# Optimization experiments

Measured on AMD Instinct MI355X. Metric: run time of the kernel, lower is better.

## Reference

```python
import jax, jax.numpy as jnp
import numpy as np
import math

N_EMBD = 1024
N_HEAD = 16
HEAD_DIM = N_EMBD // N_HEAD
SCALE = 1.0 / math.sqrt(HEAD_DIM)


def setup_inputs() -> dict:
    key = jax.random.key(0)
    ks = jax.random.split(key, 5)
    B, S = 1, 4096
    std = 0.02
    x = jax.random.normal(ks[0], (B, S, N_EMBD), dtype=jnp.float32)
    # Linear weights stored as [in, out] (transposed vs torch storage; same math)
    w_qkv = jax.random.normal(ks[1], (N_EMBD, 3 * N_EMBD), dtype=jnp.float32) * std
    b_qkv = jnp.zeros((3 * N_EMBD,), dtype=jnp.float32)
    w_out = jax.random.normal(ks[2], (N_EMBD, N_EMBD), dtype=jnp.float32) * std
    b_out = jnp.zeros((N_EMBD,), dtype=jnp.float32)
    return {"x": x, "w_qkv": w_qkv, "b_qkv": b_qkv, "w_out": w_out, "b_out": b_out}


def reference(x, w_qkv, b_qkv, w_out, b_out):
    B, S, D = x.shape
    qkv = x @ w_qkv + b_qkv                      # [B, S, 3D]
    q, k, v = jnp.split(qkv, 3, axis=-1)
    # [B, H, S, d]
    q = q.reshape(B, S, N_HEAD, HEAD_DIM).transpose(0, 2, 1, 3)
    k = k.reshape(B, S, N_HEAD, HEAD_DIM).transpose(0, 2, 1, 3)
    v = v.reshape(B, S, N_HEAD, HEAD_DIM).transpose(0, 2, 1, 3)
    scores = jnp.einsum("bhqd,bhkd->bhqk", q, k) * SCALE  # [B, H, S, S]
    causal = jnp.tril(jnp.ones((S, S), dtype=bool))
    scores = jnp.where(causal, scores, -jnp.inf)
    attn = jax.nn.softmax(scores, axis=-1)
    out = jnp.einsum("bhqk,bhkd->bhqd", attn, v)  # [B, H, S, d]
    out = out.transpose(0, 2, 1, 3).reshape(B, S, D)
    return out @ w_out + b_out
```

## Files before the change

### kernel.cpp

```cpp
#include <hip/hip_runtime.h>
#include <hip/hip_bf16.h>
#include <cstdint>

typedef __bf16 bf16x8 __attribute__((ext_vector_type(8)));
typedef float  f32x4  __attribute__((ext_vector_type(4)));

#define S_LEN 4096
#define D_EMB 1024
#define N3    3072
#define HDIM  64

__device__ __forceinline__ unsigned short f2bf(float f) {
    union { unsigned int i; float f; } v; v.f = f;
    unsigned int i = v.i;
    return (unsigned short)((i + 0x7FFFu + ((i >> 16) & 1u)) >> 16);
}

__device__ __forceinline__ void async16(const void* g, void* l) {
    __builtin_amdgcn_global_load_lds(
        (const __attribute__((address_space(1))) unsigned int*)g,
        (__attribute__((address_space(3))) unsigned int*)l,
        16, 0, 0);
}

__global__ void convert_f32_bf16(const float* __restrict__ src,
                                 unsigned short* __restrict__ dst, int n8) {
    const int i = blockIdx.x * blockDim.x + threadIdx.x;
    if (i >= n8) return;
    float4 f0 = *(const float4*)&src[i * 8];
    float4 f1 = *(const float4*)&src[i * 8 + 4];
    union { uint4 q; unsigned short s[8]; } o;
    o.s[0]=f2bf(f0.x); o.s[1]=f2bf(f0.y); o.s[2]=f2bf(f0.z); o.s[3]=f2bf(f0.w);
    o.s[4]=f2bf(f1.x); o.s[5]=f2bf(f1.y); o.s[6]=f2bf(f1.z); o.s[7]=f2bf(f1.w);
    *(uint4*)&dst[i * 8] = o.q;
}

__global__ void transpose_f32_to_bf16(const float* __restrict__ src,
                                      unsigned short* __restrict__ dst,
                                      int R, int ld, int c0) {
    __shared__ float tile[32][33];
    const int tx = threadIdx.x, ty = threadIdx.y;
    const int r0 = blockIdx.y * 32, cc0 = blockIdx.x * 32;
    for (int i = 0; i < 32; i += 8)
        tile[ty + i][tx] = src[(size_t)(r0 + ty + i) * ld + c0 + cc0 + tx];
    __syncthreads();
    for (int i = 0; i < 32; i += 8)
        dst[(size_t)(cc0 + ty + i) * R + r0 + tx] = f2bf(tile[tx][ty + i]);
}

template <int MI, bool OUT_F32, bool FUSE_VT>
__global__ __launch_bounds__(256) void gemm_bt_bias(
    const unsigned short* __restrict__ A,
    const unsigned short* __restrict__ BT,
    const float* __restrict__ bias,
    void* __restrict__ Cp,
    unsigned short* __restrict__ Vt,
    int M, int N, int K)
{
    constexpr int MTILE = MI * 32;
    constexpr int LA = MI / 2;
    __shared__ __align__(16) unsigned short As[MTILE * 32];
    __shared__ __align__(16) unsigned short Bs[128 * 32];
    const int tid  = threadIdx.x;
    const int wave = tid >> 6, lane = tid & 63;
    const int q4 = lane >> 4, l16 = lane & 15;
    const int m0 = blockIdx.y * MTILE, n0 = blockIdx.x * 128;
    const int wm = (wave >> 1) * (MI * 16), wn = (wave & 1) * 64;

    f32x4 acc[MI][4] = {};

    const int lrow = lane >> 2;
    const int scol = (lane & 3) * 8;

    for (int k0 = 0; k0 < K; k0 += 32) {
        __syncthreads();
        for (int i = 0; i < 2; ++i) {
            const int r = wave * 32 + i * 16 + lrow;
            async16(BT + (size_t)(n0 + r) * K + k0 + scol,
                    &Bs[(wave * 32 + i * 16) * 32 + lane * 8]);
        }
        for (int i = 0; i < LA; ++i) {
            const int r = wave * (16 * LA) + i * 16 + lrow;
            async16(A + (size_t)(m0 + r) * K + k0 + scol,
                    &As[(wave * (16 * LA) + i * 16) * 32 + lane * 8]);
        }
        __syncthreads();

        bf16x8 af[MI], bfr[4];
        for (int mi = 0; mi < MI; ++mi)
            af[mi] = *(const bf16x8*)&As[(wm + mi * 16 + l16) * 32 + q4 * 8];
        for (int ni = 0; ni < 4; ++ni)
            bfr[ni] = *(const bf16x8*)&Bs[(wn + ni * 16 + l16) * 32 + q4 * 8];
        for (int mi = 0; mi < MI; ++mi)
            for (int ni = 0; ni < 4; ++ni)
                acc[mi][ni] = __builtin_amdgcn_mfma_f32_16x16x32_bf16(
                    af[mi], bfr[ni], acc[mi][ni], 0, 0, 0);
    }

    if (FUSE_VT && n0 >= 2048) {
        for (int ni = 0; ni < 4; ++ni) {
            const int col = n0 + wn + ni * 16 + l16;
            const float bv = bias[col];
            const int vrow = col - 2048;
            for (int mi = 0; mi < MI; ++mi) {
                const int row = m0 + wm + mi * 16 + q4 * 4;
                union { uint2 u; unsigned short s[4]; } pk;
                for (int r = 0; r < 4; ++r) pk.s[r] = f2bf(acc[mi][ni][r] + bv);
                *(uint2*)&Vt[(size_t)vrow * S_LEN + row] = pk.u;
            }
        }
        return;
    }
    for (int ni = 0; ni < 4; ++ni) {
        const int col = n0 + wn + ni * 16 + l16;
        const float bv = bias[col];
        for (int mi = 0; mi < MI; ++mi) {
            const int row = m0 + wm + mi * 16 + q4 * 4;
            for (int r = 0; r < 4; ++r) {
                const float val = acc[mi][ni][r] + bv;
                if constexpr (OUT_F32)
                    ((float*)Cp)[(size_t)(row + r) * N + col] = val;
                else
                    ((unsigned short*)Cp)[(size_t)(row + r) * N + col] = f2bf(val);
            }
        }
    }
}

#define LDP 72
#define EXP2_SCALE 0.180336884f

__global__ __launch_bounds__(256) void attn_flash(
    const unsigned short* __restrict__ qkv,
    const unsigned short* __restrict__ Vt,
    unsigned short* __restrict__ X2)
{
    __shared__ __align__(16) unsigned short Ks[64 * LDP];
    __shared__ __align__(16) unsigned short Vs[64 * LDP];
    __shared__ __align__(16) unsigned short Ps[4 * 16 * LDP];
    const int tid  = threadIdx.x;
    const int wave = tid >> 6, lane = tid & 63;
    const int q4 = lane >> 4, l16 = lane & 15;
    const int h  = blockIdx.y;

    const int x = blockIdx.x, hg = blockIdx.y >> 2;
    int qt;
    if      (hg == 0) qt = x;
    else if (hg == 1) qt = 63 - x;
    else if (hg == 2) qt = (x + 16) & 63;
    else              qt = (47 - x) & 63;
    const int q0 = qt * 64;

    bf16x8 aq[2];
    {
        const unsigned short* qp =
            qkv + (size_t)(q0 + wave * 16 + l16) * N3 + h * HDIM + q4 * 8;
        aq[0] = *(const bf16x8*)(qp);
        aq[1] = *(const bf16x8*)(qp + 32);
    }

    float l_part[4] = {0.f, 0.f, 0.f, 0.f};
    f32x4 o[4] = {};

    const int rr = tid >> 3;
    const int cc = (tid & 7) * 8;
    unsigned short* Pw = &Ps[wave * 16 * LDP];

    for (int t = 0; t <= qt; ++t) {
        const int kv0 = t * 64;
        uint4 kv_a = *(const uint4*)&qkv[(size_t)(kv0 + rr)      * N3 + D_EMB + h * HDIM + cc];
        uint4 kv_b = *(const uint4*)&qkv[(size_t)(kv0 + 32 + rr) * N3 + D_EMB + h * HDIM + cc];
        uint4 vt_a = *(const uint4*)&Vt [(size_t)(h * HDIM + rr)      * S_LEN + kv0 + cc];
        uint4 vt_b = *(const uint4*)&Vt [(size_t)(h * HDIM + 32 + rr) * S_LEN + kv0 + cc];
        __syncthreads();
        *(uint4*)&Ks[rr * LDP + cc]        = kv_a;
        *(uint4*)&Ks[(32 + rr) * LDP + cc] = kv_b;
        *(uint4*)&Vs[rr * LDP + cc]        = vt_a;
        *(uint4*)&Vs[(32 + rr) * LDP + cc] = vt_b;
        __syncthreads();

        f32x4 sacc[4] = {};
        for (int kk = 0; kk < 2; ++kk)
            for (int nt = 0; nt < 4; ++nt) {
                bf16x8 b = *(const bf16x8*)&Ks[(nt * 16 + l16) * LDP + kk * 32 + q4 * 8];
                sacc[nt] = __builtin_amdgcn_mfma_f32_16x16x32_bf16(
                    aq[kk], b, sacc[nt], 0, 0, 0);
            }

        if (t < qt) {
            for (int r = 0; r < 4; ++r) {
                const int prow = (q4 * 4 + r) * LDP;
                for (int nt = 0; nt < 4; ++nt) {
                    float e = exp2f(sacc[nt][r] * EXP2_SCALE);
                    l_part[r] += e;
                    Pw[prow + nt * 16 + l16] =
                        (unsigned short)(__float_as_uint(e) >> 16);
                }
            }
        } else {
            for (int r = 0; r < 4; ++r) {
                const int grow = q0 + wave * 16 + q4 * 4 + r;
                const int prow = (q4 * 4 + r) * LDP;
                for (int nt = 0; nt < 4; ++nt) {
                    float e = exp2f(sacc[nt][r] * EXP2_SCALE);
                    if (kv0 + nt * 16 + l16 > grow) e = 0.f;
                    l_part[r] += e;
                    Pw[prow + nt * 16 + l16] =
                        (unsigned short)(__float_as_uint(e) >> 16);
                }
            }
        }
        __asm__ volatile("s_waitcnt lgkmcnt(0)" ::: "memory");

        for (int kk = 0; kk < 2; ++kk) {
            bf16x8 pa = *(const bf16x8*)&Pw[l16 * LDP + kk * 32 + q4 * 8];
            for (int dt = 0; dt < 4; ++dt) {
                bf16x8 vb = *(const bf16x8*)&Vs[(dt * 16 + l16) * LDP + kk * 32 + q4 * 8];
                o[dt] = __builtin_amdgcn_mfma_f32_16x16x32_bf16(pa, vb, o[dt], 0, 0, 0);
            }
        }
    }

    float linv[4];
    for (int r = 0; r < 4; ++r) {
        float l = l_part[r];
        for (int off = 1; off < 16; off <<= 1)
            l += __shfl_xor(l, off, 16);
        linv[r] = 1.f / l;
    }
    for (int dt = 0; dt < 4; ++dt)
        for (int r = 0; r < 4; ++r) {
            const int row = q0 + wave * 16 + q4 * 4 + r;
            X2[(size_t)row * D_EMB + h * HDIM + dt * 16 + l16] =
                f2bf(o[dt][r] * linv[r]);
        }
}

extern "C" void kernel_launch(void* const* d_in, const int* in_sizes, int n_in,
                              void* d_out, int out_size, void* d_ws, size_t ws_size,
                              hipStream_t stream) {
    const float* x     = (const float*)d_in[0];
    const float* w_qkv = (const float*)d_in[1];
    const float* b_qkv = (const float*)d_in[2];
    const float* w_out = (const float*)d_in[3];
    const float* b_out = (const float*)d_in[4];
    float* out = (float*)d_out;

    char* ws = (char*)d_ws;
    unsigned short* qkv   = (unsigned short*)(ws);
    unsigned short* wqkvT = (unsigned short*)(ws + 25165824);
    unsigned short* woutT = (unsigned short*)(ws + 31457280);
    unsigned short* Vt    = (unsigned short*)(ws + 33554432);
    unsigned short* X2    = (unsigned short*)(ws + 41943040);
    unsigned short* Xb    = X2;

    convert_f32_bf16<<<(4096 * 1024 / 8 + 255) / 256, 256, 0, stream>>>(
        x, Xb, 4096 * 1024 / 8);

    transpose_f32_to_bf16<<<dim3(3072 / 32, 1024 / 32), dim3(32, 8), 0, stream>>>(
        w_qkv, wqkvT, 1024, 3072, 0);
    transpose_f32_to_bf16<<<dim3(1024 / 32, 1024 / 32), dim3(32, 8), 0, stream>>>(
        w_out, woutT, 1024, 1024, 0);

    gemm_bt_bias<4, false, true><<<dim3(3072 / 128, 4096 / 128), 256, 0, stream>>>(
        Xb, wqkvT, b_qkv, qkv, Vt, 4096, 3072, 1024);

    attn_flash<<<dim3(64, 16), 256, 0, stream>>>(qkv, Vt, X2);

    gemm_bt_bias<2, true, false><<<dim3(1024 / 128, 4096 / 64), 256, 0, stream>>>(
        X2, woutT, b_out, out, nullptr, 4096, 1024, 1024);
}
```

Measured before the change: 251.6 us.

## Prefetch next K/V tile in registers, fold softmax scale into Q, split V transpose

The attention loop now loads the next K/V tile into registers right after the LDS store, so global loads overlap the QK and PV MFMAs of the current tile. The softmax scale times log2e is folded into the Q columns in the QKV GEMM epilogue, which removes one multiply per score. The fused V-transpose epilogue is dropped from the GEMM and replaced by a separate bf16 transpose kernel. That adds a kernel launch and an extra read and write of V in exchange for coalesced GEMM stores.

```diff
diff --git a/kernel.cpp b/kernel.cpp
--- a/kernel.cpp
+++ b/kernel.cpp
@@ -9,6 +9,7 @@
 #define D_EMB 1024
 #define N3    3072
 #define HDIM  64
+#define QSCALE 0.180336884f
 
 __device__ __forceinline__ unsigned short f2bf(float f) {
     union { unsigned int i; float f; } v; v.f = f;
@@ -48,13 +49,25 @@
         dst[(size_t)(cc0 + ty + i) * R + r0 + tx] = f2bf(tile[tx][ty + i]);
 }
 
-template <int MI, bool OUT_F32, bool FUSE_VT>
+__global__ void transpose_bf16(const unsigned short* __restrict__ src,
+                               unsigned short* __restrict__ dst,
+                               int R, int ld, int c0) {
+    __shared__ unsigned short tile[32][33];
+    const int tx = threadIdx.x, ty = threadIdx.y;
+    const int r0 = blockIdx.y * 32, cc0 = blockIdx.x * 32;
+    for (int i = 0; i < 32; i += 8)
+        tile[ty + i][tx] = src[(size_t)(r0 + ty + i) * ld + c0 + cc0 + tx];
+    __syncthreads();
+    for (int i = 0; i < 32; i += 8)
+        dst[(size_t)(cc0 + ty + i) * R + r0 + tx] = tile[tx][ty + i];
+}
+
+template <int MI, bool OUT_F32, bool SCALE_Q>
 __global__ __launch_bounds__(256) void gemm_bt_bias(
     const unsigned short* __restrict__ A,
     const unsigned short* __restrict__ BT,
     const float* __restrict__ bias,
     void* __restrict__ Cp,
-    unsigned short* __restrict__ Vt,
     int M, int N, int K)
 {
     constexpr int MTILE = MI * 32;
@@ -97,27 +110,14 @@
                     af[mi], bfr[ni], acc[mi][ni], 0, 0, 0);
     }
 
-    if (FUSE_VT && n0 >= 2048) {
-        for (int ni = 0; ni < 4; ++ni) {
-            const int col = n0 + wn + ni * 16 + l16;
-            const float bv = bias[col];
-            const int vrow = col - 2048;
-            for (int mi = 0; mi < MI; ++mi) {
-                const int row = m0 + wm + mi * 16 + q4 * 4;
-                union { uint2 u; unsigned short s[4]; } pk;
-                for (int r = 0; r < 4; ++r) pk.s[r] = f2bf(acc[mi][ni][r] + bv);
-                *(uint2*)&Vt[(size_t)vrow * S_LEN + row] = pk.u;
-            }
-        }
-        return;
-    }
     for (int ni = 0; ni < 4; ++ni) {
         const int col = n0 + wn + ni * 16 + l16;
         const float bv = bias[col];
+        const float sc = (SCALE_Q && col < 1024) ? QSCALE : 1.f;
         for (int mi = 0; mi < MI; ++mi) {
             const int row = m0 + wm + mi * 16 + q4 * 4;
             for (int r = 0; r < 4; ++r) {
-                const float val = acc[mi][ni][r] + bv;
+                const float val = (acc[mi][ni][r] + bv) * sc;
                 if constexpr (OUT_F32)
                     ((float*)Cp)[(size_t)(row + r) * N + col] = val;
                 else
@@ -128,8 +128,6 @@
 }
 
 #define LDP 72
-#define EXP2_SCALE 0.180336884f
-
 __global__ __launch_bounds__(256) void attn_flash(
     const unsigned short* __restrict__ qkv,
     const unsigned short* __restrict__ Vt,
@@ -166,18 +164,26 @@
     const int cc = (tid & 7) * 8;
     unsigned short* Pw = &Ps[wave * 16 * LDP];
 
+    uint4 kv_a = *(const uint4*)&qkv[(size_t)(rr)      * N3 + D_EMB + h * HDIM + cc];
+    uint4 kv_b = *(const uint4*)&qkv[(size_t)(32 + rr) * N3 + D_EMB + h * HDIM + cc];
+    uint4 vt_a = *(const uint4*)&Vt [(size_t)(h * HDIM + rr)      * S_LEN + cc];
+    uint4 vt_b = *(const uint4*)&Vt [(size_t)(h * HDIM + 32 + rr) * S_LEN + cc];
+
     for (int t = 0; t <= qt; ++t) {
-        const int kv0 = t * 64;
-        uint4 kv_a = *(const uint4*)&qkv[(size_t)(kv0 + rr)      * N3 + D_EMB + h * HDIM + cc];
-        uint4 kv_b = *(const uint4*)&qkv[(size_t)(kv0 + 32 + rr) * N3 + D_EMB + h * HDIM + cc];
-        uint4 vt_a = *(const uint4*)&Vt [(size_t)(h * HDIM + rr)      * S_LEN + kv0 + cc];
-        uint4 vt_b = *(const uint4*)&Vt [(size_t)(h * HDIM + 32 + rr) * S_LEN + kv0 + cc];
         __syncthreads();
         *(uint4*)&Ks[rr * LDP + cc]        = kv_a;
         *(uint4*)&Ks[(32 + rr) * LDP + cc] = kv_b;
         *(uint4*)&Vs[rr * LDP + cc]        = vt_a;
         *(uint4*)&Vs[(32 + rr) * LDP + cc] = vt_b;
         __syncthreads();
+
+        {
+            const int kn = (t < qt ? t + 1 : qt) * 64;
+            kv_a = *(const uint4*)&qkv[(size_t)(kn + rr)      * N3 + D_EMB + h * HDIM + cc];
+            kv_b = *(const uint4*)&qkv[(size_t)(kn + 32 + rr) * N3 + D_EMB + h * HDIM + cc];
+            vt_a = *(const uint4*)&Vt [(size_t)(h * HDIM + rr)      * S_LEN + kn + cc];
+            vt_b = *(const uint4*)&Vt [(size_t)(h * HDIM + 32 + rr) * S_LEN + kn + cc];
+        }
 
         f32x4 sacc[4] = {};
         for (int kk = 0; kk < 2; ++kk)
@@ -187,11 +193,12 @@
                     aq[kk], b, sacc[nt], 0, 0, 0);
             }
 
+        const int kv0 = t * 64;
         if (t < qt) {
             for (int r = 0; r < 4; ++r) {
                 const int prow = (q4 * 4 + r) * LDP;
                 for (int nt = 0; nt < 4; ++nt) {
-                    float e = exp2f(sacc[nt][r] * EXP2_SCALE);
+                    float e = exp2f(sacc[nt][r]);
                     l_part[r] += e;
                     Pw[prow + nt * 16 + l16] =
                         (unsigned short)(__float_as_uint(e) >> 16);
@@ -202,7 +209,7 @@
                 const int grow = q0 + wave * 16 + q4 * 4 + r;
                 const int prow = (q4 * 4 + r) * LDP;
                 for (int nt = 0; nt < 4; ++nt) {
-                    float e = exp2f(sacc[nt][r] * EXP2_SCALE);
+                    float e = exp2f(sacc[nt][r]);
                     if (kv0 + nt * 16 + l16 > grow) e = 0.f;
                     l_part[r] += e;
                     Pw[prow + nt * 16 + l16] =
@@ -263,10 +270,13 @@
         w_out, woutT, 1024, 1024, 0);
 
     gemm_bt_bias<4, false, true><<<dim3(3072 / 128, 4096 / 128), 256, 0, stream>>>(
-        Xb, wqkvT, b_qkv, qkv, Vt, 4096, 3072, 1024);
+        Xb, wqkvT, b_qkv, qkv, 4096, 3072, 1024);
+
+    transpose_bf16<<<dim3(1024 / 32, 4096 / 32), dim3(32, 8), 0, stream>>>(
+        qkv, Vt, 4096, 3072, 2048);
 
     attn_flash<<<dim3(64, 16), 256, 0, stream>>>(qkv, Vt, X2);
 
     gemm_bt_bias<2, true, false><<<dim3(1024 / 128, 4096 / 64), 256, 0, stream>>>(
-        X2, woutT, b_out, out, nullptr, 4096, 1024, 1024);
-}
+        X2, woutT, b_out, out, 4096, 1024, 1024);
+}
```

New measurement: 266.8 us. +6.1%, slower.
